# Kernel optimization log

Hardware: AMD Instinct MI355X
Metric: run time of the kernel (lower is better)

Reference implementation:

```python
import jax, jax.numpy as jnp
import numpy as np

N_NODES = 100000

def _graphconv_both(x, Wr, edges):
    # DGL GraphConv, norm='both', bias=False, allow_zero_in_degree=True:
    # out = D_in^{-1/2} * A^T_scatter( D_out^{-1/2}[src] * (X @ W)[src] )
    src, dst = edges[0], edges[1]
    ones = jnp.ones(src.shape[0], dtype=x.dtype)
    out_deg = jnp.clip(jax.ops.segment_sum(ones, src, num_segments=N_NODES), 1.0)
    in_deg = jnp.clip(jax.ops.segment_sum(ones, dst, num_segments=N_NODES), 1.0)
    norm_src = jax.lax.rsqrt(out_deg)  # [N]
    norm_dst = jax.lax.rsqrt(in_deg)   # [N]
    h = x @ Wr                          # [N, out] (mult W first since in>out)
    msg = h[src] * norm_src[src][:, None]          # [E, out]
    agg = jax.ops.segment_sum(msg, dst, num_segments=N_NODES)  # [N, out]
    return agg * norm_dst[:, None]


def setup_inputs() -> dict:
    key = jax.random.key(0)
    k1, k2, k3, k4 = jax.random.split(key, 4)
    x = jax.random.normal(k1, (N_NODES, 256), dtype=jnp.float32)
    W = jax.random.normal(k2, (4, 256, 64), dtype=jnp.float32) * 0.05
    src = jax.random.randint(k3, (4, 1, 1600000), 0, N_NODES)
    dst = jax.random.randint(k4, (4, 1, 1600000), 0, N_NODES)
    edge_index = jnp.concatenate([src, dst], axis=1).astype(jnp.int64)  # [4,2,E]
    return {"x": x, "W": W, "edge_index": edge_index}


def reference(x, W, edge_index):
    # per-relation GraphConv, stacked & summed, then tanh; dropout rate 0 -> identity
    per_rel = jax.vmap(lambda Wr, e: _graphconv_both(x, Wr, e))(W, edge_index)  # [R,N,out]
    Z = per_rel.sum(0)
    return jnp.tanh(Z)
```

## Files before the change

kernel.cpp:

```cpp
#include <hip/hip_runtime.h>
#include <hip/hip_bf16.h>

#define NN 100000
#define EPR 1600000
#define FIN 256
#define FOUT 64
#define BSZ 64
#define NB 1563
#define NBP 1568
#define CHUNK 4096
#define NBLK 391
#define EPT 16
#define CAP 4096
#define HSTRIDE ((size_t)(NN + 1) * FOUT)

typedef __attribute__((ext_vector_type(8))) short short8;
typedef __attribute__((ext_vector_type(4))) float f32x4;

__device__ __forceinline__ unsigned short f2bf(float f) {
    unsigned u = __float_as_uint(f);
    u = (u + 0x7FFFu + ((u >> 16) & 1u)) >> 16;
    return (unsigned short)u;
}
__device__ __forceinline__ float uaf(unsigned u) { return __uint_as_float(u); }

__global__ __launch_bounds__(256) void hist_all_kernel(const int* __restrict__ ei,
                                                       unsigned* __restrict__ btabD4,
                                                       unsigned* __restrict__ btabS4) {
    __shared__ unsigned hD[NB], hS[NB];
    int tid = threadIdx.x, r = blockIdx.y, blk = blockIdx.x;
    const int* src = ei + (size_t)r * 2 * EPR;
    const int* dst = src + EPR;
    for (int i = tid; i < NB; i += 256) { hD[i] = 0; hS[i] = 0; }
    __syncthreads();
    int e0 = blk * CHUNK;
    #pragma unroll
    for (int t = 0; t < EPT; ++t) {
        int e = e0 + t * 256 + tid;
        if (e < EPR) {
            atomicAdd(&hS[src[e] >> 6], 1u);
            atomicAdd(&hD[dst[e] >> 6], 1u);
        }
    }
    __syncthreads();
    size_t row = ((size_t)r * NBLK + blk) * NBP;
    for (int i = tid; i < NB; i += 256) {
        btabD4[row + i] = hD[i];
        btabS4[row + i] = hS[i];
    }
}

__global__ __launch_bounds__(256) void btot_all_kernel(unsigned* __restrict__ btabD4,
                                                       unsigned* __restrict__ btabS4,
                                                       unsigned* __restrict__ totD4,
                                                       unsigned* __restrict__ totS4) {
    int r = blockIdx.z;
    unsigned* tab = (blockIdx.y ? btabS4 : btabD4) + (size_t)r * NBLK * NBP;
    unsigned* tot = (blockIdx.y ? totS4 : totD4) + (size_t)r * NBP;
    __shared__ unsigned tile[NBLK][8];
    int b0 = blockIdx.x * 8;
    for (int idx = threadIdx.x; idx < NBLK * 8; idx += 256) {
        int blk = idx >> 3, bb = idx & 7;
        int b = b0 + bb;
        tile[blk][bb] = (b < NB) ? tab[(size_t)blk * NBP + b] : 0u;
    }
    __syncthreads();
    if (threadIdx.x < 8) {
        int bb = threadIdx.x;
        unsigned s = 0;
        for (int blk = 0; blk < NBLK; ++blk) {
            unsigned v = tile[blk][bb];
            tile[blk][bb] = s;
            s += v;
        }
        if (b0 + bb < NB) tot[b0 + bb] = s;
    }
    __syncthreads();
    for (int idx = threadIdx.x; idx < NBLK * 8; idx += 256) {
        int blk = idx >> 3, bb = idx & 7;
        int b = b0 + bb;
        if (b < NB) tab[(size_t)blk * NBP + b] = tile[blk][bb];
    }
}

__global__ void scan_all_kernel(const unsigned* __restrict__ totD4, const unsigned* __restrict__ totS4,
                                unsigned* __restrict__ gbaseD4, unsigned* __restrict__ gbaseS4) {
    int r = blockIdx.y;
    const unsigned* tot = (blockIdx.x ? totS4 : totD4) + (size_t)r * NBP;
    unsigned* gb = (blockIdx.x ? gbaseS4 : gbaseD4) + (size_t)r * NBP;
    __shared__ unsigned sc[256];
    int tid = threadIdx.x;
    unsigned loc[8]; unsigned s = 0;
    #pragma unroll
    for (int k = 0; k < 8; ++k) {
        int idx = tid * 8 + k;
        unsigned v = (idx < NB) ? tot[idx] : 0u;
        loc[k] = s; s += v;
    }
    sc[tid] = s; __syncthreads();
    for (int off = 1; off < 256; off <<= 1) {
        unsigned a = (tid >= off) ? sc[tid - off] : 0u;
        __syncthreads(); sc[tid] += a; __syncthreads();
    }
    unsigned texcl = tid ? sc[tid - 1] : 0u;
    #pragma unroll
    for (int k = 0; k < 8; ++k) {
        int idx = tid * 8 + k;
        if (idx < NB) gb[idx] = texcl + loc[k];
    }
}

__global__ __launch_bounds__(256) void placeD_all_kernel(const int* __restrict__ ei,
                                                         const unsigned* __restrict__ gbaseD4,
                                                         const unsigned* __restrict__ btabD4,
                                                         unsigned* __restrict__ pairs4) {
    __shared__ unsigned h[NB], hloc[NB], hbase[NB], sc[256];
    __shared__ unsigned buf[CHUNK], buf2[CHUNK];
    int tid = threadIdx.x, blk = blockIdx.x, r = blockIdx.y;
    const int* src = ei + (size_t)r * 2 * EPR;
    const int* dst = src + EPR;
    const unsigned* gbase = gbaseD4 + (size_t)r * NBP;
    const unsigned* pblk = btabD4 + ((size_t)r * NBLK + blk) * NBP;
    unsigned* pairs = pairs4 + (size_t)r * EPR;
    int e0 = blk * CHUNK;
    int csize = EPR - e0; if (csize > CHUNK) csize = CHUNK;

    for (int i = tid; i < NB; i += 256) h[i] = 0;
    __syncthreads();

    int es[EPT], ed[EPT];
    #pragma unroll
    for (int t = 0; t < EPT; ++t) {
        int e = e0 + t * 256 + tid;
        if (e < EPR) { es[t] = src[e]; ed[t] = dst[e]; atomicAdd(&h[ed[t] >> 6], 1u); }
        else { es[t] = -1; ed[t] = 0; }
    }
    __syncthreads();

    unsigned loc[8]; unsigned s = 0;
    #pragma unroll
    for (int k = 0; k < 8; ++k) {
        int idx = tid * 8 + k;
        unsigned v = (idx < NB) ? h[idx] : 0u;
        loc[k] = s; s += v;
    }
    sc[tid] = s; __syncthreads();
    for (int off = 1; off < 256; off <<= 1) {
        unsigned a = (tid >= off) ? sc[tid - off] : 0u;
        __syncthreads(); sc[tid] += a; __syncthreads();
    }
    unsigned texcl = tid ? sc[tid - 1] : 0u;
    #pragma unroll
    for (int k = 0; k < 8; ++k) {
        int idx = tid * 8 + k;
        if (idx < NB) hloc[idx] = texcl + loc[k];
    }
    __syncthreads();

    for (int i = tid; i < NB; i += 256) hbase[i] = gbase[i] + pblk[i];
    __syncthreads();
    for (int i = tid; i < NB; i += 256) h[i] = 0;
    __syncthreads();

    #pragma unroll
    for (int t = 0; t < EPT; ++t) {
        if (es[t] >= 0) {
            int b = ed[t] >> 6;
            unsigned rr = atomicAdd(&h[b], 1u);
            unsigned slot = hloc[b] + rr;
            buf[slot] = (unsigned)es[t] | ((unsigned)(ed[t] & 63) << 17);
            buf2[slot] = hbase[b] + rr;
        }
    }
    __syncthreads();

    for (int k = tid; k < csize; k += 256)
        pairs[buf2[k]] = buf[k];
}

__global__ __launch_bounds__(256) void placeS_all_kernel(const int* __restrict__ ei,
                                                         const unsigned* __restrict__ gbaseS4,
                                                         const unsigned* __restrict__ btabS4,
                                                         unsigned char* __restrict__ pairs2_4) {
    __shared__ unsigned h[NB], hloc[NB], hbase[NB], sc[256];
    __shared__ unsigned char bufB[CHUNK];
    __shared__ unsigned buf2[CHUNK];
    int tid = threadIdx.x, blk = blockIdx.x, r = blockIdx.y;
    const int* src = ei + (size_t)r * 2 * EPR;
    const unsigned* gbase = gbaseS4 + (size_t)r * NBP;
    const unsigned* pblk = btabS4 + ((size_t)r * NBLK + blk) * NBP;
    unsigned char* pairs2 = pairs2_4 + (size_t)r * EPR;
    int e0 = blk * CHUNK;
    int csize = EPR - e0; if (csize > CHUNK) csize = CHUNK;

    for (int i = tid; i < NB; i += 256) h[i] = 0;
    __syncthreads();

    int es[EPT];
    #pragma unroll
    for (int t = 0; t < EPT; ++t) {
        int e = e0 + t * 256 + tid;
        if (e < EPR) { es[t] = src[e]; atomicAdd(&h[es[t] >> 6], 1u); }
        else es[t] = -1;
    }
    __syncthreads();

    unsigned loc[8]; unsigned s = 0;
    #pragma unroll
    for (int k = 0; k < 8; ++k) {
        int idx = tid * 8 + k;
        unsigned v = (idx < NB) ? h[idx] : 0u;
        loc[k] = s; s += v;
    }
    sc[tid] = s; __syncthreads();
    for (int off = 1; off < 256; off <<= 1) {
        unsigned a = (tid >= off) ? sc[tid - off] : 0u;
        __syncthreads(); sc[tid] += a; __syncthreads();
    }
    unsigned texcl = tid ? sc[tid - 1] : 0u;
    #pragma unroll
    for (int k = 0; k < 8; ++k) {
        int idx = tid * 8 + k;
        if (idx < NB) hloc[idx] = texcl + loc[k];
    }
    __syncthreads();

    for (int i = tid; i < NB; i += 256) hbase[i] = gbase[i] + pblk[i];
    __syncthreads();
    for (int i = tid; i < NB; i += 256) h[i] = 0;
    __syncthreads();

    #pragma unroll
    for (int t = 0; t < EPT; ++t) {
        if (es[t] >= 0) {
            int b = es[t] >> 6;
            unsigned rr = atomicAdd(&h[b], 1u);
            unsigned slot = hloc[b] + rr;
            bufB[slot] = (unsigned char)(es[t] & 63);
            buf2[slot] = hbase[b] + rr;
        }
    }
    __syncthreads();

    for (int k = tid; k < csize; k += 256)
        pairs2[buf2[k]] = bufB[k];
}

__global__ void srcdeg_all_kernel(const unsigned char* __restrict__ pairs2_4,
                                  const unsigned* __restrict__ gbaseS4,
                                  const unsigned* __restrict__ totS4,
                                  float* __restrict__ nsb4) {
    __shared__ unsigned cnt[BSZ];
    int tid = threadIdx.x, b = blockIdx.x, r = blockIdx.y;
    const unsigned char* pairs2 = pairs2_4 + (size_t)r * EPR;
    if (tid < BSZ) cnt[tid] = 0;
    __syncthreads();
    unsigned st = gbaseS4[(size_t)r * NBP + b];
    int n = (int)totS4[(size_t)r * NBP + b];
    for (int i = tid; i < n; i += 256)
        atomicAdd(&cnt[pairs2[st + i]], 1u);
    __syncthreads();
    if (tid < BSZ) {
        int node = b * BSZ + tid;
        if (node < NN) {
            unsigned c = cnt[tid]; if (c < 1u) c = 1u;
            nsb4[(size_t)r * NN + node] = rsqrtf((float)c);
        }
    }
}

__global__ __launch_bounds__(256, 2) void gemm4_kernel(const float* __restrict__ x,
                                                       const float* __restrict__ W,
                                                       unsigned short* __restrict__ hsb4,
                                                       const float* __restrict__ nsb4) {
    __shared__ unsigned short xs[128][40];
    __shared__ unsigned short wt[4][64][40];
    int tid = threadIdx.x;
    int wave = tid >> 6, lane = tid & 63;
    int wm = (wave >> 1) * 64;
    int wn = (wave & 1) * 32;
    int m0 = blockIdx.x * 128;

    f32x4 acc[4][4][2];
    #pragma unroll
    for (int r = 0; r < 4; ++r)
        #pragma unroll
        for (int mi = 0; mi < 4; ++mi)
            #pragma unroll
            for (int ni = 0; ni < 2; ++ni)
                acc[r][mi][ni] = (f32x4){0.f, 0.f, 0.f, 0.f};

    int srow = tid >> 1, skp = (tid & 1) * 16;
    int swn = tid >> 2, skq = (tid & 3) * 8;
    int gr = m0 + srow; if (gr >= NN) gr = NN - 1;
    const float* xrow = &x[(size_t)gr * FIN];

    for (int k0 = 0; k0 < FIN; k0 += 32) {
        #pragma unroll
        for (int q = 0; q < 4; ++q) {
            float4 v = *(const float4*)(xrow + k0 + skp + q * 4);
            unsigned lo = (unsigned)f2bf(v.x) | ((unsigned)f2bf(v.y) << 16);
            unsigned hi = (unsigned)f2bf(v.z) | ((unsigned)f2bf(v.w) << 16);
            *(uint2*)&xs[srow][skp + q * 4] = make_uint2(lo, hi);
        }
        #pragma unroll
        for (int r = 0; r < 4; ++r) {
            const float* w = W + (size_t)r * FIN * FOUT;
            unsigned pk[4];
            #pragma unroll
            for (int i = 0; i < 8; i += 2) {
                unsigned short b0 = f2bf(w[(size_t)(k0 + skq + i) * FOUT + swn]);
                unsigned short b1 = f2bf(w[(size_t)(k0 + skq + i + 1) * FOUT + swn]);
                pk[i >> 1] = (unsigned)b0 | ((unsigned)b1 << 16);
            }
            *(uint4*)&wt[r][swn][skq] = make_uint4(pk[0], pk[1], pk[2], pk[3]);
        }
        __syncthreads();

        int fr = lane & 15, fk = (lane >> 4) * 8;
        short8 af[4];
        #pragma unroll
        for (int mi = 0; mi < 4; ++mi) af[mi] = *(const short8*)&xs[wm + mi * 16 + fr][fk];
        #pragma unroll
        for (int r = 0; r < 4; ++r) {
            short8 b0 = *(const short8*)&wt[r][wn + fr][fk];
            short8 b1 = *(const short8*)&wt[r][wn + 16 + fr][fk];
            #pragma unroll
            for (int mi = 0; mi < 4; ++mi) {
                acc[r][mi][0] = __builtin_amdgcn_mfma_f32_16x16x32_bf16(af[mi], b0, acc[r][mi][0], 0, 0, 0);
                acc[r][mi][1] = __builtin_amdgcn_mfma_f32_16x16x32_bf16(af[mi], b1, acc[r][mi][1], 0, 0, 0);
            }
        }
        __syncthreads();
    }

    int fr = lane & 15, frow4 = (lane >> 4) * 4;
    #pragma unroll
    for (int r = 0; r < 4; ++r) {
        unsigned short* hsb = hsb4 + (size_t)r * HSTRIDE;
        const float* ns = nsb4 + (size_t)r * NN;
        #pragma unroll
        for (int mi = 0; mi < 4; ++mi) {
            #pragma unroll
            for (int rg = 0; rg < 4; ++rg) {
                int grow = m0 + wm + mi * 16 + frow4 + rg;
                if (grow < NN) {
                    float sc2 = ns[grow];
                    #pragma unroll
                    for (int ni = 0; ni < 2; ++ni) {
                        int gcol = wn + ni * 16 + fr;
                        hsb[(size_t)grow * FOUT + gcol] = f2bf(acc[r][mi][ni][rg] * sc2);
                    }
                }
            }
        }
    }
    if (blockIdx.x == 0 && tid < FOUT) {
        #pragma unroll
        for (int r = 0; r < 4; ++r)
            hsb4[(size_t)r * HSTRIDE + (size_t)NN * FOUT + tid] = 0;
    }
}

__global__ __launch_bounds__(512, 4) void aggsort4_kernel(const unsigned* __restrict__ pairs4,
                                                          const unsigned* __restrict__ gbaseD4,
                                                          const unsigned* __restrict__ totD4,
                                                          const unsigned short* __restrict__ hsb4,
                                                          float* __restrict__ out) {
    __shared__ unsigned sorted[CAP];
    __shared__ unsigned cnt[BSZ];
    __shared__ unsigned tdeg[BSZ];
    __shared__ unsigned loff[BSZ + 1];
    int tid = threadIdx.x;
    int b = blockIdx.x;
    int wave = tid >> 6, lane = tid & 63;
    int lg = lane >> 4;
    int lp = lane & 15;
    const unsigned DUMMY = (unsigned)NN;

    f32x4 acc4[8];
    #pragma unroll
    for (int i = 0; i < 8; ++i) acc4[i] = (f32x4){0.f, 0.f, 0.f, 0.f};

    for (int r = 0; r < 4; ++r) {
        const unsigned* pairs = pairs4 + (size_t)r * EPR;
        const char* hsbB = (const char*)(hsb4 + (size_t)r * HSTRIDE) + (lp << 3);
        unsigned start = gbaseD4[(size_t)r * NBP + b];
        int n = (int)totD4[(size_t)r * NBP + b];

        __syncthreads();
        if (tid < BSZ) cnt[tid] = 0;
        __syncthreads();

        if (n <= CAP - 960) {
            unsigned rec[CAP / 512];
            #pragma unroll
            for (int t = 0; t < CAP / 512; ++t) {
                int i = t * 512 + tid;
                rec[t] = 0xFFFFFFFFu;
                if (i < n) {
                    rec[t] = pairs[start + i];
                    atomicAdd(&cnt[rec[t] >> 17], 1u);
                }
            }
            __syncthreads();
            if (wave == 0) {
                unsigned v = cnt[lane];
                unsigned pad = (v + 15u) & ~15u;
                unsigned sum = pad;
                #pragma unroll
                for (int o = 1; o < 64; o <<= 1) {
                    unsigned u = __shfl_up(sum, o);
                    if (lane >= o) sum += u;
                }
                loff[lane + 1] = sum;
                if (lane == 0) loff[0] = 0;
                tdeg[lane] = v;
                cnt[lane] = sum - pad;
            }
            __syncthreads();
            int ptot = (int)loff[BSZ];
            for (int i = tid; i < ptot; i += 512) sorted[i] = DUMMY;
            __syncthreads();
            #pragma unroll
            for (int t = 0; t < CAP / 512; ++t) {
                if (rec[t] != 0xFFFFFFFFu) {
                    unsigned p = atomicAdd(&cnt[rec[t] >> 17], 1u);
                    sorted[p] = rec[t];
                }
            }
            __syncthreads();

            #pragma unroll
            for (int i = 0; i < 8; ++i) {
                int nl = wave * 8 + i;
                int node = b * BSZ + nl;
                if (node >= NN) break;
                int lo = (int)loff[nl], hi = (int)loff[nl + 1];
                f32x4 seg = (f32x4){0.f, 0.f, 0.f, 0.f};
                for (int j0 = lo; j0 < hi; j0 += 16) {
                    unsigned q0 = sorted[j0 + lg];
                    unsigned q1 = sorted[j0 + 4 + lg];
                    unsigned q2 = sorted[j0 + 8 + lg];
                    unsigned q3 = sorted[j0 + 12 + lg];
                    uint2 u0 = *(const uint2*)(hsbB + (((size_t)(q0 & 0x1FFFF)) << 7));
                    uint2 u1 = *(const uint2*)(hsbB + (((size_t)(q1 & 0x1FFFF)) << 7));
                    uint2 u2 = *(const uint2*)(hsbB + (((size_t)(q2 & 0x1FFFF)) << 7));
                    uint2 u3 = *(const uint2*)(hsbB + (((size_t)(q3 & 0x1FFFF)) << 7));
                    seg.x += uaf(u0.x << 16); seg.y += uaf(u0.x & 0xFFFF0000u);
                    seg.z += uaf(u0.y << 16); seg.w += uaf(u0.y & 0xFFFF0000u);
                    seg.x += uaf(u1.x << 16); seg.y += uaf(u1.x & 0xFFFF0000u);
                    seg.z += uaf(u1.y << 16); seg.w += uaf(u1.y & 0xFFFF0000u);
                    seg.x += uaf(u2.x << 16); seg.y += uaf(u2.x & 0xFFFF0000u);
                    seg.z += uaf(u2.y << 16); seg.w += uaf(u2.y & 0xFFFF0000u);
                    seg.x += uaf(u3.x << 16); seg.y += uaf(u3.x & 0xFFFF0000u);
                    seg.z += uaf(u3.y << 16); seg.w += uaf(u3.y & 0xFFFF0000u);
                }
                unsigned d = tdeg[nl]; if (d < 1u) d = 1u;
                float ndv = rsqrtf((float)d);
                acc4[i].x += seg.x * ndv;
                acc4[i].y += seg.y * ndv;
                acc4[i].z += seg.z * ndv;
                acc4[i].w += seg.w * ndv;
            }
        } else {
            for (int i = 0; i < 8; ++i) {
                int nl = wave * 8 + i;
                int node = b * BSZ + nl;
                if (node >= NN) break;
                f32x4 seg = (f32x4){0.f, 0.f, 0.f, 0.f};
                int deg = 0;
                for (int j = 0; j < n; ++j) {
                    unsigned q = pairs[start + j];
                    if ((int)(q >> 17) == nl) {
                        uint2 u = *(const uint2*)(hsbB + (((size_t)(q & 0x1FFFF)) << 7));
                        seg.x += uaf(u.x << 16);
                        seg.y += uaf(u.x & 0xFFFF0000u);
                        seg.z += uaf(u.y << 16);
                        seg.w += uaf(u.y & 0xFFFF0000u);
                        ++deg;
                    }
                }
                if (deg < 1) deg = 1;
                float ndv = rsqrtf((float)deg) * 0.25f;
                acc4[i].x += seg.x * ndv;
                acc4[i].y += seg.y * ndv;
                acc4[i].z += seg.z * ndv;
                acc4[i].w += seg.w * ndv;
            }
        }
    }

    #pragma unroll
    for (int i = 0; i < 8; ++i) {
        int nl = wave * 8 + i;
        int node = b * BSZ + nl;
        f32x4 v = acc4[i];
        v.x += __shfl_xor(v.x, 16); v.y += __shfl_xor(v.y, 16);
        v.z += __shfl_xor(v.z, 16); v.w += __shfl_xor(v.w, 16);
        v.x += __shfl_xor(v.x, 32); v.y += __shfl_xor(v.y, 32);
        v.z += __shfl_xor(v.z, 32); v.w += __shfl_xor(v.w, 32);
        if (node < NN && lg == 0) {
            float4 o;
            o.x = tanhf(v.x); o.y = tanhf(v.y); o.z = tanhf(v.z); o.w = tanhf(v.w);
            *(float4*)&out[(size_t)node * FOUT + lp * 4] = o;
        }
    }
}

extern "C" void kernel_launch(void* const* d_in, const int* in_sizes, int n_in,
                              void* d_out, int out_size, void* d_ws, size_t ws_size,
                              hipStream_t stream) {
    const float* x = (const float*)d_in[0];
    const float* W = (const float*)d_in[1];
    const int* ei = (const int*)d_in[2];
    float* out = (float*)d_out;

    char* ws = (char*)d_ws;
    size_t o = 0;
    unsigned short* hsb4 = (unsigned short*)(ws + o); o += (size_t)4 * HSTRIDE * 2;
    unsigned* pairs4 = (unsigned*)(ws + o);   o += (size_t)4 * EPR * 4;
    unsigned char* pairs2_4 = (unsigned char*)(ws + o); o += (size_t)4 * EPR;
    unsigned* btabD4 = (unsigned*)(ws + o);   o += (size_t)4 * NBLK * NBP * 4;
    unsigned* btabS4 = (unsigned*)(ws + o);   o += (size_t)4 * NBLK * NBP * 4;
    unsigned* totD4 = (unsigned*)(ws + o);    o += (size_t)4 * NBP * 4;
    unsigned* totS4 = (unsigned*)(ws + o);    o += (size_t)4 * NBP * 4;
    unsigned* gbaseD4 = (unsigned*)(ws + o);  o += (size_t)4 * NBP * 4;
    unsigned* gbaseS4 = (unsigned*)(ws + o);  o += (size_t)4 * NBP * 4;
    float* nsb4 = (float*)(ws + o);           o += (size_t)4 * NN * 4;

    hist_all_kernel<<<dim3(NBLK, 4), 256, 0, stream>>>(ei, btabD4, btabS4);
    btot_all_kernel<<<dim3((NB + 7) / 8, 2, 4), 256, 0, stream>>>(btabD4, btabS4, totD4, totS4);
    scan_all_kernel<<<dim3(2, 4), 256, 0, stream>>>(totD4, totS4, gbaseD4, gbaseS4);
    placeD_all_kernel<<<dim3(NBLK, 4), 256, 0, stream>>>(ei, gbaseD4, btabD4, pairs4);
    placeS_all_kernel<<<dim3(NBLK, 4), 256, 0, stream>>>(ei, gbaseS4, btabS4, pairs2_4);
    srcdeg_all_kernel<<<dim3(NB, 4), 256, 0, stream>>>(pairs2_4, gbaseS4, totS4, nsb4);
    gemm4_kernel<<<(NN + 127) / 128, 256, 0, stream>>>(x, W, hsb4, nsb4);
    aggsort4_kernel<<<NB, 512, 0, stream>>>(pairs4, gbaseD4, totD4, hsb4, out);
}
```

Measured before the change: 409.5 us.

## Interleave two node segments in aggregation, pre-shift pair offsets, simplify column scan

The aggregation loop now walks two destination nodes' edge segments together, issuing eight independent gathers per iteration instead of four to raise memory-level parallelism. Packed pair records now store the source row already shifted to a byte offset, with the local node id in the top byte, which removes a shift from the gather address calculation. The per-bucket column scan is rewritten so each thread scans one bucket directly in global memory instead of staging a tile in shared memory. Pairing nodes can waste lanes when the two degrees differ, and the new encoding relies on the shifted offsets fitting in 24 bits.

After: 451.7 us. +10.3%, slower.

```diff
diff --git a/kernel.cpp b/kernel.cpp
--- a/kernel.cpp
+++ b/kernel.cpp
@@ -23,6 +23,10 @@
     return (unsigned short)u;
 }
 __device__ __forceinline__ float uaf(unsigned u) { return __uint_as_float(u); }
+__device__ __forceinline__ void unpk(f32x4& seg, uint2 u) {
+    seg.x += uaf(u.x << 16); seg.y += uaf(u.x & 0xFFFF0000u);
+    seg.z += uaf(u.y << 16); seg.w += uaf(u.y & 0xFFFF0000u);
+}
 
 __global__ __launch_bounds__(256) void hist_all_kernel(const int* __restrict__ ei,
                                                        unsigned* __restrict__ btabD4,
@@ -50,37 +54,24 @@
     }
 }
 
-__global__ __launch_bounds__(256) void btot_all_kernel(unsigned* __restrict__ btabD4,
-                                                       unsigned* __restrict__ btabS4,
-                                                       unsigned* __restrict__ totD4,
-                                                       unsigned* __restrict__ totS4) {
+__global__ __launch_bounds__(64) void btot_all_kernel(unsigned* __restrict__ btabD4,
+                                                      unsigned* __restrict__ btabS4,
+                                                      unsigned* __restrict__ totD4,
+                                                      unsigned* __restrict__ totS4) {
     int r = blockIdx.z;
     unsigned* tab = (blockIdx.y ? btabS4 : btabD4) + (size_t)r * NBLK * NBP;
     unsigned* tot = (blockIdx.y ? totS4 : totD4) + (size_t)r * NBP;
-    __shared__ unsigned tile[NBLK][8];
-    int b0 = blockIdx.x * 8;
-    for (int idx = threadIdx.x; idx < NBLK * 8; idx += 256) {
-        int blk = idx >> 3, bb = idx & 7;
-        int b = b0 + bb;
-        tile[blk][bb] = (b < NB) ? tab[(size_t)blk * NBP + b] : 0u;
-    }
-    __syncthreads();
-    if (threadIdx.x < 8) {
-        int bb = threadIdx.x;
-        unsigned s = 0;
-        for (int blk = 0; blk < NBLK; ++blk) {
-            unsigned v = tile[blk][bb];
-            tile[blk][bb] = s;
-            s += v;
-        }
-        if (b0 + bb < NB) tot[b0 + bb] = s;
-    }
-    __syncthreads();
-    for (int idx = threadIdx.x; idx < NBLK * 8; idx += 256) {
-        int blk = idx >> 3, bb = idx & 7;
-        int b = b0 + bb;
-        if (b < NB) tab[(size_t)blk * NBP + b] = tile[blk][bb];
-    }
+    int b = blockIdx.x * 64 + threadIdx.x;
+    if (b >= NB) return;
+    unsigned s = 0;
+    #pragma unroll 4
+    for (int blk = 0; blk < NBLK; ++blk) {
+        size_t idx = (size_t)blk * NBP + b;
+        unsigned v = tab[idx];
+        tab[idx] = s;
+        s += v;
+    }
+    tot[b] = s;
 }
 
 __global__ void scan_all_kernel(const unsigned* __restrict__ totD4, const unsigned* __restrict__ totS4,
@@ -168,7 +159,7 @@
             int b = ed[t] >> 6;
             unsigned rr = atomicAdd(&h[b], 1u);
             unsigned slot = hloc[b] + rr;
-            buf[slot] = (unsigned)es[t] | ((unsigned)(ed[t] & 63) << 17);
+            buf[slot] = ((unsigned)es[t] << 7) | ((unsigned)(ed[t] & 63) << 24);
             buf2[slot] = hbase[b] + rr;
         }
     }
@@ -376,7 +367,7 @@
     int wave = tid >> 6, lane = tid & 63;
     int lg = lane >> 4;
     int lp = lane & 15;
-    const unsigned DUMMY = (unsigned)NN;
+    const unsigned DUMMY = (unsigned)NN << 7;
 
     f32x4 acc4[8];
     #pragma unroll
@@ -400,7 +391,7 @@
                 rec[t] = 0xFFFFFFFFu;
                 if (i < n) {
                     rec[t] = pairs[start + i];
-                    atomicAdd(&cnt[rec[t] >> 17], 1u);
+                    atomicAdd(&cnt[rec[t] >> 24], 1u);
                 }
             }
             __syncthreads();
@@ -425,43 +416,61 @@
             #pragma unroll
             for (int t = 0; t < CAP / 512; ++t) {
                 if (rec[t] != 0xFFFFFFFFu) {
-                    unsigned p = atomicAdd(&cnt[rec[t] >> 17], 1u);
+                    unsigned p = atomicAdd(&cnt[rec[t] >> 24], 1u);
                     sorted[p] = rec[t];
                 }
             }
             __syncthreads();
 
             #pragma unroll
-            for (int i = 0; i < 8; ++i) {
-                int nl = wave * 8 + i;
-                int node = b * BSZ + nl;
-                if (node >= NN) break;
-                int lo = (int)loff[nl], hi = (int)loff[nl + 1];
-                f32x4 seg = (f32x4){0.f, 0.f, 0.f, 0.f};
-                for (int j0 = lo; j0 < hi; j0 += 16) {
-                    unsigned q0 = sorted[j0 + lg];
-                    unsigned q1 = sorted[j0 + 4 + lg];
-                    unsigned q2 = sorted[j0 + 8 + lg];
-                    unsigned q3 = sorted[j0 + 12 + lg];
-                    uint2 u0 = *(const uint2*)(hsbB + (((size_t)(q0 & 0x1FFFF)) << 7));
-                    uint2 u1 = *(const uint2*)(hsbB + (((size_t)(q1 & 0x1FFFF)) << 7));
-                    uint2 u2 = *(const uint2*)(hsbB + (((size_t)(q2 & 0x1FFFF)) << 7));
-                    uint2 u3 = *(const uint2*)(hsbB + (((size_t)(q3 & 0x1FFFF)) << 7));
-                    seg.x += uaf(u0.x << 16); seg.y += uaf(u0.x & 0xFFFF0000u);
-                    seg.z += uaf(u0.y << 16); seg.w += uaf(u0.y & 0xFFFF0000u);
-                    seg.x += uaf(u1.x << 16); seg.y += uaf(u1.x & 0xFFFF0000u);
-                    seg.z += uaf(u1.y << 16); seg.w += uaf(u1.y & 0xFFFF0000u);
-                    seg.x += uaf(u2.x << 16); seg.y += uaf(u2.x & 0xFFFF0000u);
-                    seg.z += uaf(u2.y << 16); seg.w += uaf(u2.y & 0xFFFF0000u);
-                    seg.x += uaf(u3.x << 16); seg.y += uaf(u3.x & 0xFFFF0000u);
-                    seg.z += uaf(u3.y << 16); seg.w += uaf(u3.y & 0xFFFF0000u);
-                }
-                unsigned d = tdeg[nl]; if (d < 1u) d = 1u;
-                float ndv = rsqrtf((float)d);
-                acc4[i].x += seg.x * ndv;
-                acc4[i].y += seg.y * ndv;
-                acc4[i].z += seg.z * ndv;
-                acc4[i].w += seg.w * ndv;
+            for (int i = 0; i < 8; i += 2) {
+                int nlA = wave * 8 + i;
+                int nodeA = b * BSZ + nlA;
+                if (nodeA >= NN) break;
+                bool haveB = (nodeA + 1) < NN;
+                int jA = (int)loff[nlA];
+                int hiA = (int)loff[nlA + 1];
+                int jB = hiA;
+                int hiB = haveB ? (int)loff[nlA + 2] : hiA;
+                f32x4 segA = (f32x4){0.f, 0.f, 0.f, 0.f};
+                f32x4 segB = (f32x4){0.f, 0.f, 0.f, 0.f};
+                while ((jA < hiA) || (jB < hiB)) {
+                    bool hA = jA < hiA, hB = jB < hiB;
+                    int ja = hA ? jA : 0;
+                    int jb = hB ? jB : 0;
+                    unsigned qa0 = sorted[ja + lg],      qb0 = sorted[jb + lg];
+                    unsigned qa1 = sorted[ja + 4 + lg],  qb1 = sorted[jb + 4 + lg];
+                    unsigned qa2 = sorted[ja + 8 + lg],  qb2 = sorted[jb + 8 + lg];
+                    unsigned qa3 = sorted[ja + 12 + lg], qb3 = sorted[jb + 12 + lg];
+                    uint2 a0 = *(const uint2*)(hsbB + (qa0 & 0xFFFFFFu));
+                    uint2 a1 = *(const uint2*)(hsbB + (qa1 & 0xFFFFFFu));
+                    uint2 a2 = *(const uint2*)(hsbB + (qa2 & 0xFFFFFFu));
+                    uint2 a3 = *(const uint2*)(hsbB + (qa3 & 0xFFFFFFu));
+                    uint2 b0 = *(const uint2*)(hsbB + (qb0 & 0xFFFFFFu));
+                    uint2 b1 = *(const uint2*)(hsbB + (qb1 & 0xFFFFFFu));
+                    uint2 b2 = *(const uint2*)(hsbB + (qb2 & 0xFFFFFFu));
+                    uint2 b3 = *(const uint2*)(hsbB + (qb3 & 0xFFFFFFu));
+                    if (hA) {
+                        unpk(segA, a0); unpk(segA, a1); unpk(segA, a2); unpk(segA, a3);
+                        jA += 16;
+                    }
+                    if (hB) {
+                        unpk(segB, b0); unpk(segB, b1); unpk(segB, b2); unpk(segB, b3);
+                        jB += 16;
+                    }
+                }
+                {
+                    unsigned d = tdeg[nlA]; if (d < 1u) d = 1u;
+                    float nv = rsqrtf((float)d);
+                    acc4[i].x += segA.x * nv; acc4[i].y += segA.y * nv;
+                    acc4[i].z += segA.z * nv; acc4[i].w += segA.w * nv;
+                }
+                if (haveB) {
+                    unsigned d = tdeg[nlA + 1]; if (d < 1u) d = 1u;
+                    float nv = rsqrtf((float)d);
+                    acc4[i + 1].x += segB.x * nv; acc4[i + 1].y += segB.y * nv;
+                    acc4[i + 1].z += segB.z * nv; acc4[i + 1].w += segB.w * nv;
+                }
             }
         } else {
             for (int i = 0; i < 8; ++i) {
@@ -472,21 +481,16 @@
                 int deg = 0;
                 for (int j = 0; j < n; ++j) {
                     unsigned q = pairs[start + j];
-                    if ((int)(q >> 17) == nl) {
-                        uint2 u = *(const uint2*)(hsbB + (((size_t)(q & 0x1FFFF)) << 7));
-                        seg.x += uaf(u.x << 16);
-                        seg.y += uaf(u.x & 0xFFFF0000u);
-                        seg.z += uaf(u.y << 16);
-                        seg.w += uaf(u.y & 0xFFFF0000u);
+                    if ((int)(q >> 24) == nl) {
+                        uint2 u = *(const uint2*)(hsbB + (q & 0xFFFFFFu));
+                        unpk(seg, u);
                         ++deg;
                     }
                 }
                 if (deg < 1) deg = 1;
-                float ndv = rsqrtf((float)deg) * 0.25f;
-                acc4[i].x += seg.x * ndv;
-                acc4[i].y += seg.y * ndv;
-                acc4[i].z += seg.z * ndv;
-                acc4[i].w += seg.w * ndv;
+                float nv = rsqrtf((float)deg) * 0.25f;
+                acc4[i].x += seg.x * nv; acc4[i].y += seg.y * nv;
+                acc4[i].z += seg.z * nv; acc4[i].w += seg.w * nv;
             }
         }
     }
@@ -530,7 +534,7 @@
     float* nsb4 = (float*)(ws + o);           o += (size_t)4 * NN * 4;
 
     hist_all_kernel<<<dim3(NBLK, 4), 256, 0, stream>>>(ei, btabD4, btabS4);
-    btot_all_kernel<<<dim3((NB + 7) / 8, 2, 4), 256, 0, stream>>>(btabD4, btabS4, totD4, totS4);
+    btot_all_kernel<<<dim3((NB + 63) / 64, 2, 4), 64, 0, stream>>>(btabD4, btabS4, totD4, totS4);
     scan_all_kernel<<<dim3(2, 4), 256, 0, stream>>>(totD4, totS4, gbaseD4, gbaseS4);
     placeD_all_kernel<<<dim3(NBLK, 4), 256, 0, stream>>>(ei, gbaseD4, btabD4, pairs4);
     placeS_all_kernel<<<dim3(NBLK, 4), 256, 0, stream>>>(ei, gbaseS4, btabS4, pairs2_4);
```
